# Kernel tuning notes

Hardware: AMD Instinct MI355X
Metric: run time of the kernel (lower is better)

Reference implementation:

```python
import jax, jax.numpy as jnp
import numpy as np

BATCH = 32768


def _unpack(packed, n):
    # packed: [rows, ceil(n/8)] ints in [0,256). Extract bits MSB-first per byte.
    bits = (packed[:, :, None] >> jnp.arange(7, -1, -1, dtype=packed.dtype)) & 1
    return bits.reshape(packed.shape[0], -1)[:, :n]  # [rows, n] of {0,1}


def setup_inputs() -> dict:
    key = jax.random.key(0)
    k0, k1, k2, k3, k4 = jax.random.split(key, 5)
    return {
        "x": jax.random.normal(k0, (BATCH, 784), dtype=jnp.float32),
        "w1_packed": jax.random.randint(k1, (256, 98), 0, 256, dtype=jnp.int32),
        "m1_packed": jax.random.randint(k2, (256, 98), 0, 256, dtype=jnp.int32),
        "alpha1": jnp.float32(1.0),
        "w2_packed": jax.random.randint(k3, (10, 32), 0, 256, dtype=jnp.int32),
        "m2_packed": jax.random.randint(k4, (10, 32), 0, 256, dtype=jnp.int32),
        "alpha2": jnp.float32(1.0),
    }


def reference(x, w1_packed, m1_packed, alpha1, w2_packed, m2_packed, alpha2):
    # Layer 1: binary {-1,+1} weights * {0,1} mask * alpha
    w1 = (2 * _unpack(w1_packed, 784) - 1).astype(jnp.float32)
    w1 = w1 * _unpack(m1_packed, 784).astype(jnp.float32) * alpha1  # [256, 784]
    h = jax.nn.relu(jnp.einsum('bi,oi->bo', x, w1))  # [B, 256]
    # Layer 2
    w2 = (2 * _unpack(w2_packed, 256) - 1).astype(jnp.float32)
    w2 = w2 * _unpack(m2_packed, 256).astype(jnp.float32) * alpha2  # [10, 256]
    return jnp.einsum('bh,oh->bo', h, w2)  # [B, 10]
```

## Files before the change

kernel.cpp:

```cpp
#include <hip/hip_runtime.h>
#include <hip/hip_bf16.h>

typedef __bf16 bf16x8 __attribute__((ext_vector_type(8)));
typedef float floatx4 __attribute__((ext_vector_type(4)));

#define GLB_AS __attribute__((address_space(1)))
#define LDS_AS __attribute__((address_space(3)))

__device__ __forceinline__ void async_cp16(const void* g, void* l) {
  __builtin_amdgcn_global_load_lds((GLB_AS void*)g, (LDS_AS void*)l, 16, 0, 0);
}

__device__ __forceinline__ unsigned short f2bf(float f) {
  __bf16 b = (__bf16)f;
  return __builtin_bit_cast(unsigned short, b);
}

__global__ void decode_w1_kernel(const int* __restrict__ w1p,
                                 const int* __restrict__ m1p,
                                 unsigned short* __restrict__ w1t) {
  int t = blockIdx.x * 256 + threadIdx.x;
  int r = t & 255;
  int j = t >> 8;
  unsigned short vals[8];
#pragma unroll
  for (int k = 0; k < 8; ++k) vals[k] = 0;
  if (j < 98) {
    unsigned int v = (unsigned int)w1p[r * 98 + j];
    unsigned int m = (unsigned int)m1p[r * 98 + j];
#pragma unroll
    for (int k = 0; k < 8; ++k) {
      unsigned int bit = (v >> (7 - k)) & 1u;
      unsigned int mk  = (m >> (7 - k)) & 1u;
      vals[k] = (unsigned short)(mk ? (bit ? 0x3F80u : 0xBF80u) : 0u);
    }
  }
  uint4 pack;
  pack.x = (unsigned)vals[0] | ((unsigned)vals[1] << 16);
  pack.y = (unsigned)vals[2] | ((unsigned)vals[3] << 16);
  pack.z = (unsigned)vals[4] | ((unsigned)vals[5] << 16);
  pack.w = (unsigned)vals[6] | ((unsigned)vals[7] << 16);
  *reinterpret_cast<uint4*>(w1t + t * 8) = pack;
}

#define BM 64
#define BK 32
#define NCH 25
#define HS_LD 264
#define W2_LD 264

#define OFF_WS0 0
#define OFF_WS1 8192
#define OFF_XS0 16384
#define OFF_XS1 18432
#define OFF_HS  0
#define OFF_W2  16896

__global__ __launch_bounds__(512, 4) void fused_kernel(
    const float* __restrict__ x,
    const unsigned short* __restrict__ w1t,
    const int* __restrict__ w2p,
    const int* __restrict__ m2p,
    const float* __restrict__ a1p,
    const float* __restrict__ a2p,
    float* __restrict__ out) {
  __shared__ unsigned short smem[64 * HS_LD + 16 * W2_LD];

  const int tid  = threadIdx.x;
  const int wave = tid >> 6;
  const int lane = tid & 63;
  const int l15  = lane & 15;
  const int quad = lane >> 4;
  const int row0 = blockIdx.x * BM;

  floatx4 acc[4][2];
#pragma unroll
  for (int i = 0; i < 4; ++i)
#pragma unroll
    for (int j = 0; j < 2; ++j) acc[i][j] = (floatx4){0.f, 0.f, 0.f, 0.f};

  const int xr  = tid >> 3;
  const int xc4 = tid & 7;
  const int xq  = xc4 >> 1;
  const int xh  = xc4 & 1;
  const float* xbase = x + (size_t)(row0 + xr) * 784 + xc4 * 4;
  const int xs_off = (xq * 64 + xr) * 8 + xh * 4;

  auto stage_w = [&](int kc, int offW) {
#pragma unroll
    for (int it = 0; it < 2; ++it) {
      int seg = it * 512 + tid;
      async_cp16(w1t + (size_t)kc * 8192 + seg * 8, &smem[offW + seg * 8]);
    }
  };
  auto load_x = [&](int kc, float4& xv) {
    int col = kc * BK + xc4 * 4;
    if (col < 784) {
      xv = *reinterpret_cast<const float4*>(xbase + kc * BK);
    } else {
      xv = (float4){0.f, 0.f, 0.f, 0.f};
    }
  };
  auto cvt_write = [&](int offX, const float4& xv) {
    ushort4 b;
    b.x = f2bf(xv.x); b.y = f2bf(xv.y); b.z = f2bf(xv.z); b.w = f2bf(xv.w);
    *reinterpret_cast<ushort4*>(&smem[offX + xs_off]) = b;
  };
  auto compute = [&](int offW, int offX) {
    bf16x8 af[4], bfr[2];
#pragma unroll
    for (int mi = 0; mi < 4; ++mi)
      af[mi] = *reinterpret_cast<const bf16x8*>(
          &smem[offX + (quad * 64 + mi * 16 + l15) * 8]);
#pragma unroll
    for (int nj = 0; nj < 2; ++nj)
      bfr[nj] = *reinterpret_cast<const bf16x8*>(
          &smem[offW + (quad * 256 + wave * 32 + nj * 16 + l15) * 8]);
#pragma unroll
    for (int mi = 0; mi < 4; ++mi)
#pragma unroll
      for (int nj = 0; nj < 2; ++nj)
        acc[mi][nj] = __builtin_amdgcn_mfma_f32_16x16x32_bf16(
            af[mi], bfr[nj], acc[mi][nj], 0, 0, 0);
  };

  {
    float4 xv;
    load_x(0, xv);
    stage_w(0, OFF_WS0);
    cvt_write(OFF_XS0, xv);
  }
  __syncthreads();

#pragma unroll 2
  for (int kc = 0; kc < NCH - 1; ++kc) {
    const int p = kc & 1;
    float4 xn;
    load_x(kc + 1, xn);
    stage_w(kc + 1, p ? OFF_WS0 : OFF_WS1);
    compute(p ? OFF_WS1 : OFF_WS0,
            p ? OFF_XS1 : OFF_XS0);
    cvt_write(p ? OFF_XS0 : OFF_XS1, xn);
    __syncthreads();
  }
  compute(OFF_WS0, OFF_XS0);
  __syncthreads();

  const float a1 = a1p[0];
  const float a2 = a2p[0];
#pragma unroll
  for (int mi = 0; mi < 4; ++mi) {
#pragma unroll
    for (int nj = 0; nj < 2; ++nj) {
      int col   = wave * 32 + nj * 16 + l15;
      int rbase = mi * 16 + quad * 4;
#pragma unroll
      for (int r = 0; r < 4; ++r) {
        float h = fmaxf(a1 * acc[mi][nj][r], 0.f);
        smem[OFF_HS + (rbase + r) * HS_LD + col] = f2bf(h);
      }
    }
  }
  if (tid < 320) {
    int r = tid >> 5, j = tid & 31;
    unsigned int v = (unsigned int)w2p[r * 32 + j];
    unsigned int m = (unsigned int)m2p[r * 32 + j];
#pragma unroll
    for (int k = 0; k < 8; ++k) {
      unsigned int bit = (v >> (7 - k)) & 1u;
      unsigned int mk  = (m >> (7 - k)) & 1u;
      smem[OFF_W2 + r * W2_LD + j * 8 + k] =
          (unsigned short)(mk ? (bit ? 0x3F80u : 0xBF80u) : 0u);
    }
  }
  for (int idx = tid; idx < 6 * 256; idx += 512) {
    int r = 10 + (idx >> 8), c = idx & 255;
    smem[OFF_W2 + r * W2_LD + c] = 0;
  }
  __syncthreads();

  if (wave < 4) {
    floatx4 o2 = (floatx4){0.f, 0.f, 0.f, 0.f};
#pragma unroll
    for (int ks = 0; ks < 8; ++ks) {
      bf16x8 ha = *reinterpret_cast<const bf16x8*>(
          &smem[OFF_HS + (wave * 16 + l15) * HS_LD + ks * 32 + quad * 8]);
      bf16x8 wb = *reinterpret_cast<const bf16x8*>(
          &smem[OFF_W2 + l15 * W2_LD + ks * 32 + quad * 8]);
      o2 = __builtin_amdgcn_mfma_f32_16x16x32_bf16(ha, wb, o2, 0, 0, 0);
    }
    if (l15 < 10) {
#pragma unroll
      for (int r = 0; r < 4; ++r) {
        int gr = row0 + wave * 16 + quad * 4 + r;
        out[(size_t)gr * 10 + l15] = a2 * o2[r];
      }
    }
  }
}

extern "C" void kernel_launch(void* const* d_in, const int* in_sizes, int n_in,
                              void* d_out, int out_size, void* d_ws, size_t ws_size,
                              hipStream_t stream) {
  const float* x   = (const float*)d_in[0];
  const int*   w1p = (const int*)d_in[1];
  const int*   m1p = (const int*)d_in[2];
  const float* a1  = (const float*)d_in[3];
  const int*   w2p = (const int*)d_in[4];
  const int*   m2p = (const int*)d_in[5];
  const float* a2  = (const float*)d_in[6];
  unsigned short* w1t = (unsigned short*)d_ws;
  float* out = (float*)d_out;

  decode_w1_kernel<<<100, 256, 0, stream>>>(w1p, m1p, w1t);
  fused_kernel<<<512, 512, 0, stream>>>(x, w1t, w2p, m2p, a1, a2, out);
}
```

Before: 171.7 us.

## Stage x in two large superphases and read W1 fragments directly from global

Replaces the 25-step double-buffered K loop with two superphases. Each superphase converts and stores 416 columns of x into LDS behind a single barrier, then runs 13 MFMA steps with register double-buffered fragments. W1 B-fragments are now loaded straight from global (L2-resident) rather than staged through LDS with async copies, which removes most of the per-chunk barriers. The cost is less overlap between x global loads and compute, since all loads are issued before each superphase, and more global traffic for W1. The decode grid grows so W1 is zero-padded to 832 columns.

```diff
diff --git a/kernel.cpp b/kernel.cpp
--- a/kernel.cpp
+++ b/kernel.cpp
@@ -3,13 +3,6 @@
 
 typedef __bf16 bf16x8 __attribute__((ext_vector_type(8)));
 typedef float floatx4 __attribute__((ext_vector_type(4)));
-
-#define GLB_AS __attribute__((address_space(1)))
-#define LDS_AS __attribute__((address_space(3)))
-
-__device__ __forceinline__ void async_cp16(const void* g, void* l) {
-  __builtin_amdgcn_global_load_lds((GLB_AS void*)g, (LDS_AS void*)l, 16, 0, 0);
-}
 
 __device__ __forceinline__ unsigned short f2bf(float f) {
   __bf16 b = (__bf16)f;
@@ -44,17 +37,12 @@
 }
 
 #define BM 64
-#define BK 32
-#define NCH 25
+#define NCHG 26
+#define NCHP 13
 #define HS_LD 264
 #define W2_LD 264
 
-#define OFF_WS0 0
-#define OFF_WS1 8192
-#define OFF_XS0 16384
-#define OFF_XS1 18432
-#define OFF_HS  0
-#define OFF_W2  16896
+#define OFF_W2 16896
 
 __global__ __launch_bounds__(512, 4) void fused_kernel(
     const float* __restrict__ x,
@@ -64,7 +52,7 @@
     const float* __restrict__ a1p,
     const float* __restrict__ a2p,
     float* __restrict__ out) {
-  __shared__ unsigned short smem[64 * HS_LD + 16 * W2_LD];
+  __shared__ unsigned short smem[26624];
 
   const int tid  = threadIdx.x;
   const int wave = tid >> 6;
@@ -79,72 +67,91 @@
 #pragma unroll
     for (int j = 0; j < 2; ++j) acc[i][j] = (floatx4){0.f, 0.f, 0.f, 0.f};
 
-  const int xr  = tid >> 3;
-  const int xc4 = tid & 7;
-  const int xq  = xc4 >> 1;
-  const int xh  = xc4 & 1;
-  const float* xbase = x + (size_t)(row0 + xr) * 784 + xc4 * 4;
-  const int xs_off = (xq * 64 + xr) * 8 + xh * 4;
-
-  auto stage_w = [&](int kc, int offW) {
-#pragma unroll
-    for (int it = 0; it < 2; ++it) {
-      int seg = it * 512 + tid;
-      async_cp16(w1t + (size_t)kc * 8192 + seg * 8, &smem[offW + seg * 8]);
-    }
-  };
-  auto load_x = [&](int kc, float4& xv) {
-    int col = kc * BK + xc4 * 4;
-    if (col < 784) {
-      xv = *reinterpret_cast<const float4*>(xbase + kc * BK);
-    } else {
-      xv = (float4){0.f, 0.f, 0.f, 0.f};
-    }
-  };
-  auto cvt_write = [&](int offX, const float4& xv) {
-    ushort4 b;
-    b.x = f2bf(xv.x); b.y = f2bf(xv.y); b.z = f2bf(xv.z); b.w = f2bf(xv.w);
-    *reinterpret_cast<ushort4*>(&smem[offX + xs_off]) = b;
-  };
-  auto compute = [&](int offW, int offX) {
-    bf16x8 af[4], bfr[2];
+  const unsigned short* wl = w1t + ((size_t)wave * 32 + l15) * 8;
+
+  auto ldfrags = [&](int cg, int cl, bf16x8* af, bf16x8* bfv) {
 #pragma unroll
     for (int mi = 0; mi < 4; ++mi)
       af[mi] = *reinterpret_cast<const bf16x8*>(
-          &smem[offX + (quad * 64 + mi * 16 + l15) * 8]);
+          &smem[((cl * 4 + quad) * 64 + mi * 16 + l15) * 8]);
 #pragma unroll
     for (int nj = 0; nj < 2; ++nj)
-      bfr[nj] = *reinterpret_cast<const bf16x8*>(
-          &smem[offW + (quad * 256 + wave * 32 + nj * 16 + l15) * 8]);
+      bfv[nj] = *reinterpret_cast<const bf16x8*>(
+          wl + (size_t)(cg * 4 + quad) * 2048 + nj * 128);
+  };
+  auto mm = [&](bf16x8* af, bf16x8* bfv) {
 #pragma unroll
     for (int mi = 0; mi < 4; ++mi)
 #pragma unroll
       for (int nj = 0; nj < 2; ++nj)
         acc[mi][nj] = __builtin_amdgcn_mfma_f32_16x16x32_bf16(
-            af[mi], bfr[nj], acc[mi][nj], 0, 0, 0);
+            af[mi], bfv[nj], acc[mi][nj], 0, 0, 0);
   };
 
-  {
-    float4 xv;
-    load_x(0, xv);
-    stage_w(0, OFF_WS0);
-    cvt_write(OFF_XS0, xv);
-  }
-  __syncthreads();
-
-#pragma unroll 2
-  for (int kc = 0; kc < NCH - 1; ++kc) {
-    const int p = kc & 1;
-    float4 xn;
-    load_x(kc + 1, xn);
-    stage_w(kc + 1, p ? OFF_WS0 : OFF_WS1);
-    compute(p ? OFF_WS1 : OFF_WS0,
-            p ? OFF_XS1 : OFF_XS0);
-    cvt_write(p ? OFF_XS0 : OFF_XS1, xn);
+  auto superphase = [&](const int sp) {
+    const int r  = tid >> 3;
+    const int g0 = tid & 7;
+    {
+      float4 xv[7];
+#pragma unroll
+      for (int it = 0; it < 7; ++it) {
+        int g = g0 + it * 8;
+        int col = sp * 416 + g * 4;
+        if (col < 784)
+          xv[it] = *reinterpret_cast<const float4*>(
+              x + (size_t)(row0 + r) * 784 + col);
+        else
+          xv[it] = (float4){0.f, 0.f, 0.f, 0.f};
+      }
+#pragma unroll
+      for (int it = 0; it < 7; ++it) {
+        int g = g0 + it * 8;
+        ushort4 b;
+        b.x = f2bf(xv[it].x); b.y = f2bf(xv[it].y);
+        b.z = f2bf(xv[it].z); b.w = f2bf(xv[it].w);
+        *reinterpret_cast<ushort4*>(&smem[((g >> 1) * 64 + r) * 8 + (g & 1) * 4]) = b;
+      }
+    }
+    {
+      float4 xv[6];
+#pragma unroll
+      for (int it = 0; it < 6; ++it) {
+        int g = g0 + 56 + it * 8;
+        int col = sp * 416 + g * 4;
+        if (col < 784)
+          xv[it] = *reinterpret_cast<const float4*>(
+              x + (size_t)(row0 + r) * 784 + col);
+        else
+          xv[it] = (float4){0.f, 0.f, 0.f, 0.f};
+      }
+#pragma unroll
+      for (int it = 0; it < 6; ++it) {
+        int g = g0 + 56 + it * 8;
+        ushort4 b;
+        b.x = f2bf(xv[it].x); b.y = f2bf(xv[it].y);
+        b.z = f2bf(xv[it].z); b.w = f2bf(xv[it].w);
+        *reinterpret_cast<ushort4*>(&smem[((g >> 1) * 64 + r) * 8 + (g & 1) * 4]) = b;
+      }
+    }
     __syncthreads();
-  }
-  compute(OFF_WS0, OFF_XS0);
-  __syncthreads();
+
+    bf16x8 afA[4], bfA[2], afB[4], bfB[2];
+    ldfrags(sp * NCHP, 0, afA, bfA);
+#pragma unroll
+    for (int cl = 0; cl < NCHP; ++cl) {
+      if ((cl & 1) == 0) {
+        if (cl < NCHP - 1) ldfrags(sp * NCHP + cl + 1, cl + 1, afB, bfB);
+        mm(afA, bfA);
+      } else {
+        if (cl < NCHP - 1) ldfrags(sp * NCHP + cl + 1, cl + 1, afA, bfA);
+        mm(afB, bfB);
+      }
+    }
+    __syncthreads();
+  };
+
+  superphase(0);
+  superphase(1);
 
   const float a1 = a1p[0];
   const float a2 = a2p[0];
@@ -157,7 +164,7 @@
 #pragma unroll
       for (int r = 0; r < 4; ++r) {
         float h = fmaxf(a1 * acc[mi][nj][r], 0.f);
-        smem[OFF_HS + (rbase + r) * HS_LD + col] = f2bf(h);
+        smem[(rbase + r) * HS_LD + col] = f2bf(h);
       }
     }
   }
@@ -184,7 +191,7 @@
 #pragma unroll
     for (int ks = 0; ks < 8; ++ks) {
       bf16x8 ha = *reinterpret_cast<const bf16x8*>(
-          &smem[OFF_HS + (wave * 16 + l15) * HS_LD + ks * 32 + quad * 8]);
+          &smem[(wave * 16 + l15) * HS_LD + ks * 32 + quad * 8]);
       bf16x8 wb = *reinterpret_cast<const bf16x8*>(
           &smem[OFF_W2 + l15 * W2_LD + ks * 32 + quad * 8]);
       o2 = __builtin_amdgcn_mfma_f32_16x16x32_bf16(ha, wb, o2, 0, 0, 0);
@@ -212,6 +219,6 @@
   unsigned short* w1t = (unsigned short*)d_ws;
   float* out = (float*)d_out;
 
-  decode_w1_kernel<<<100, 256, 0, stream>>>(w1p, m1p, w1t);
+  decode_w1_kernel<<<104, 256, 0, stream>>>(w1p, m1p, w1t);
   fused_kernel<<<512, 512, 0, stream>>>(x, w1t, w2p, m2p, a1, a2, out);
 }
```

Result: no change. 170.9 us (-0.5%).
